# Optimization experiments

Measured on AMD Instinct MI355X. Metric: run time of the kernel, lower is better.

Reference implementation:

```python
import jax, jax.numpy as jnp
import numpy as np

H, K, V, F = 8, 64, 192, 192  # heads, key_size, value_size, num_position_features


def central_mask_features(distances, feature_size, seq_length):
    # distances: [L] float; returns [L, feature_size]
    pow_rate = np.exp(np.log(seq_length + 1) / feature_size).astype('float32')
    center_widths = jnp.power(pow_rate, jnp.arange(1, feature_size + 1, dtype=jnp.float32)) - 1.0
    return (center_widths[None, :] > jnp.abs(distances)[:, None]).astype(jnp.float32)


def positional_features(distances, feature_size, seq_length, symmetric=False):
    num_components = 1 if symmetric else 2
    emb = central_mask_features(distances, feature_size // num_components, seq_length)
    if not symmetric:
        emb = jnp.concatenate([emb, jnp.sign(distances)[:, None] * emb], axis=-1)
    return emb  # [L, feature_size]


def relative_shift(x):
    # x: [B, H, T1, T2] with T2 = 2*T1 - 1 -> [B, H, T1, T1]
    b, h, t1, t2 = x.shape
    x = jnp.pad(x, ((0, 0), (0, 0), (0, 0), (1, 0)))  # [B,H,T1,T2+1]
    x = x.reshape(b, h, t2 + 1, t1)[:, :, 1:, :]      # drop first row
    x = x.reshape(b, h, t1, t2)
    return x[..., : (t2 + 1) // 2]


def setup_inputs() -> dict:
    key = jax.random.key(0)
    ks = jax.random.split(key, 9)
    B, T, C = 2, 1536, 1536
    s = 1.0 / np.sqrt(C).astype('float32')
    return {
        'inputs': jax.random.normal(ks[0], (B, T, C), jnp.float32),
        'Wq': jax.random.normal(ks[1], (C, H * K), jnp.float32) * s,
        'Wk': jax.random.normal(ks[2], (C, H * K), jnp.float32) * s,
        'Wv': jax.random.normal(ks[3], (C, H * V), jnp.float32) * s,
        'Wrk': jax.random.normal(ks[4], (F, H * K), jnp.float32) * (1.0 / np.sqrt(F).astype('float32')),
        'We': jax.random.normal(ks[5], (H * V, H * V), jnp.float32) * (1.0 / np.sqrt(H * V).astype('float32')),
        'be': jnp.zeros((H * V,), jnp.float32),
        'r_w_bias': jax.random.normal(ks[6], (1, H, 1, K), jnp.float32) * 0.1,
        'r_r_bias': jax.random.normal(ks[7], (1, H, 1, K), jnp.float32) * 0.1,
    }


def reference(inputs, Wq, Wk, Wv, Wrk, We, be, r_w_bias, r_r_bias):
    B, T, C = inputs.shape

    def heads(x, d):  # [B,T,H*d] -> [B,H,T,d]
        return x.reshape(B, T, H, d).transpose(0, 2, 1, 3)

    q = heads(inputs @ Wq, K) * (K ** -0.5)
    k = heads(inputs @ Wk, K)
    v = heads(inputs @ Wv, V)

    # content logits: (q + r_w_bias) k^T -> [B,H,T,T]
    content_logits = jnp.einsum('bhqk,bhmk->bhqm', q + r_w_bias, k)

    # relative position logits
    distances = jnp.arange(-T + 1, T, dtype=jnp.float32)  # [2T-1]
    pe = positional_features(distances, F, T, symmetric=False)  # [2T-1, F]
    r_k = (pe @ Wrk).reshape(2 * T - 1, H, K).transpose(1, 0, 2)  # [H, 2T-1, K]
    rel_logits = jnp.einsum('bhqk,hmk->bhqm', q + r_r_bias, r_k)  # [B,H,T,2T-1]
    rel_logits = relative_shift(rel_logits)  # [B,H,T,T]

    logits = content_logits + rel_logits
    attn = jax.nn.softmax(logits, axis=-1)
    out = jnp.einsum('bhqm,bhmv->bhqv', attn, v)  # [B,H,T,V]
    out = out.transpose(0, 2, 1, 3).reshape(B, T, H * V)
    return out @ We + be
```

## Files before the change

kernel.cpp:

```cpp
#include <hip/hip_runtime.h>
#include <math.h>

#define HB 8
#define KD 64
#define VD 192
#define BT 2
#define TT 1536
#define CC 1536
#define HK (HB*KD)
#define HV (HB*VD)
#define QKVP 2560
#define LOG2E 1.44269504088896340736f

typedef float f32x4 __attribute__((ext_vector_type(4)));
typedef __bf16 bf16x8 __attribute__((ext_vector_type(8)));

static __device__ __forceinline__ ushort f2bf(float f) {
  union { float f; uint u; } v; v.f = f;
  uint r = (v.u + 0x7FFFu + ((v.u >> 16) & 1u)) >> 16;
  return (ushort)r;
}
static __device__ __forceinline__ float bf2f(ushort u) {
  union { uint u; float f; } v; v.u = ((uint)u) << 16; return v.f;
}

static __device__ __forceinline__ f32x4 mfma_bf(bf16x8 a, bf16x8 b, f32x4 c) {
  return __builtin_amdgcn_mfma_f32_16x16x32_bf16(a, b, c, 0, 0, 0);
}

static __device__ __forceinline__ void gload_lds16(const ushort* g, ushort* l) {
  __builtin_amdgcn_global_load_lds(
      (const __attribute__((address_space(1))) unsigned int*)g,
      (__attribute__((address_space(3))) unsigned int*)l, 16, 0, 0);
}

__device__ __forceinline__ void storeC(float* p, float v) { *p = v; }
__device__ __forceinline__ void storeC(ushort* p, float v) { *p = f2bf(v); }

__global__ __launch_bounds__(256) void cast_bf16(
    const float* __restrict__ in, ushort* __restrict__ out, int n4)
{
  for (int i = blockIdx.x*blockDim.x + threadIdx.x; i < n4; i += gridDim.x*blockDim.x) {
    float4 v = ((const float4*)in)[i];
    ushort4 o; o.x = f2bf(v.x); o.y = f2bf(v.y); o.z = f2bf(v.z); o.w = f2bf(v.w);
    ((ushort4*)out)[i] = o;
  }
}

__global__ void tcast(const float* __restrict__ in, ushort* __restrict__ out, int R, int C, float scale)
{
  __shared__ float tile[32][33];
  const int bx = blockIdx.x * 32;
  const int by = blockIdx.y * 32;
  const int tx = threadIdx.x, ty = threadIdx.y;
  #pragma unroll
  for (int i = 0; i < 4; ++i)
    tile[ty + i*8][tx] = in[(size_t)(by + ty + i*8)*C + bx + tx];
  __syncthreads();
  #pragma unroll
  for (int i = 0; i < 4; ++i)
    out[(size_t)(bx + ty + i*8)*R + by + tx] = f2bf(tile[tx][ty + i*8] * scale);
}

__global__ void vtrans(const ushort* __restrict__ in, ushort* __restrict__ out)
{
  __shared__ ushort tile[32][33];
  const int bx = blockIdx.x * 32;
  const int by = blockIdx.y * 32;
  const int tx = threadIdx.x, ty = threadIdx.y;
  #pragma unroll
  for (int i = 0; i < 4; ++i)
    tile[ty + i*8][tx] = in[(size_t)(by + ty + i*8)*QKVP + 1024 + bx + tx];
  __syncthreads();
  #pragma unroll
  for (int i = 0; i < 4; ++i)
    out[(size_t)(bx + ty + i*8)*(BT*TT) + by + tx] = tile[tx][ty + i*8];
}

template<bool WITH_BIAS, typename OutT>
__global__ __launch_bounds__(256) void gemm_bf16(
    const ushort* __restrict__ A, const ushort* __restrict__ Bt,
    const float* __restrict__ bias, OutT* __restrict__ C,
    int M, int N, int Kd)
{
  __shared__ __align__(16) ushort As[128*64];
  __shared__ __align__(16) ushort Bs[128*64];
  const int t = threadIdx.x;
  const int w = t >> 6, lane = t & 63;
  const int lrow = lane & 15, lk8 = lane >> 4;
  const int row0 = blockIdx.y * 128, col0 = blockIdx.x * 128;
  const int wr = (w >> 1) * 64, wc = (w & 1) * 64;

  f32x4 acc[4][4];
  #pragma unroll
  for (int m = 0; m < 4; ++m)
    #pragma unroll
    for (int n = 0; n < 4; ++n) acc[m][n] = (f32x4){0.f,0.f,0.f,0.f};

  for (int k0 = 0; k0 < Kd; k0 += 64) {
    __syncthreads();
    #pragma unroll
    for (int j = 0; j < 4; ++j) {
      const int c = (w*4 + j)*64 + lane;
      const int r = c >> 3, cp = c & 7;
      const int sc = cp ^ (r & 7);
      gload_lds16(A  + (size_t)(row0 + r)*Kd + k0 + sc*8, As + c*8);
      gload_lds16(Bt + (size_t)(col0 + r)*Kd + k0 + sc*8, Bs + c*8);
    }
    __syncthreads();
    bf16x8 af[4][2], bfv[4][2];
    #pragma unroll
    for (int m = 0; m < 4; ++m) {
      const int r = wr + m*16 + lrow;
      #pragma unroll
      for (int kh = 0; kh < 2; ++kh) {
        const int k8 = lk8 + kh*4;
        af[m][kh] = *(const bf16x8*)&As[r*64 + ((k8 ^ (r & 7)) << 3)];
      }
    }
    #pragma unroll
    for (int n = 0; n < 4; ++n) {
      const int r = wc + n*16 + lrow;
      #pragma unroll
      for (int kh = 0; kh < 2; ++kh) {
        const int k8 = lk8 + kh*4;
        bfv[n][kh] = *(const bf16x8*)&Bs[r*64 + ((k8 ^ (r & 7)) << 3)];
      }
    }
    #pragma unroll
    for (int m = 0; m < 4; ++m)
      #pragma unroll
      for (int n = 0; n < 4; ++n) {
        acc[m][n] = mfma_bf(af[m][0], bfv[n][0], acc[m][n]);
        acc[m][n] = mfma_bf(af[m][1], bfv[n][1], acc[m][n]);
      }
  }
  #pragma unroll
  for (int m = 0; m < 4; ++m)
    #pragma unroll
    for (int n = 0; n < 4; ++n) {
      const int cg = col0 + wc + n*16 + lrow;
      const float bb = WITH_BIAS ? bias[cg] : 0.f;
      #pragma unroll
      for (int r = 0; r < 4; ++r) {
        const int rg = row0 + wr + m*16 + lk8*4 + r;
        storeC(&C[(size_t)rg*N + cg], acc[m][n][r] + bb);
      }
    }
}

__global__ __launch_bounds__(256) void wrk_suffix(
    const float* __restrict__ Wrk, float* __restrict__ S1, float* __restrict__ S2)
{
  const int c = blockIdx.x*blockDim.x + threadIdx.x;
  float a1 = 0.f, a2 = 0.f;
  S1[96*HK + c] = 0.f; S2[96*HK + c] = 0.f;
  for (int i = 95; i >= 0; --i) {
    a1 += Wrk[i*HK + c];
    a2 += Wrk[(96 + i)*HK + c];
    S1[i*HK + c] = a1; S2[i*HK + c] = a2;
  }
}

__global__ __launch_bounds__(256) void relk_fill(
    const float* __restrict__ S1, const float* __restrict__ S2,
    const float* __restrict__ rrb, ushort* __restrict__ rk, float* __restrict__ c2g)
{
  __shared__ float cw[96];
  __shared__ float red[512];
  __shared__ int i0s;
  const int t = threadIdx.x;
  const int m = blockIdx.x;
  if (t < 96) {
    double pr = exp(log((double)(TT + 1)) / 96.0);
    float prf = (float)pr;
    cw[t] = (float)pow((double)prf, (double)(t + 1)) - 1.0f;
  }
  __syncthreads();
  const int d = m - (TT - 1);
  const float ad = fabsf((float)d);
  if (t == 0) {
    int i0 = 96;
    for (int i = 0; i < 96; ++i) if (cw[i] > ad) { i0 = i; break; }
    i0s = i0;
  }
  __syncthreads();
  const float sg = (d > 0) ? 1.f : (d < 0 ? -1.f : 0.f);
  const int i0 = i0s;
  for (int c = t; c < HK; c += 256) {
    const float val = S1[i0*HK + c] + sg * S2[i0*HK + c];
    const ushort vb = f2bf(val);
    rk[(size_t)m * HK + c] = vb;
    red[c] = bf2f(vb) * rrb[c];
  }
  __syncthreads();
  if (t < 8) {
    float s = 0.f;
    #pragma unroll 16
    for (int i = 0; i < 64; ++i) s += red[t*64 + i];
    c2g[(size_t)t*(2*TT - 1) + m] = s * LOG2E;
  }
}

__global__ __launch_bounds__(256) void c1_kernel(
    const ushort* __restrict__ qkv, const float* __restrict__ rwb, float* __restrict__ c1g)
{
  const int idx = blockIdx.x*256 + threadIdx.x;
  const int h = idx & 7, row = idx >> 3;
  const ushort* kr = &qkv[(size_t)row*QKVP + 512 + h*KD];
  float s = 0.f;
  #pragma unroll 16
  for (int c = 0; c < 64; ++c) s += bf2f(kr[c]) * rwb[h*KD + c];
  c1g[h*(BT*TT) + row] = s * LOG2E;
}

__global__ __launch_bounds__(256, 2) void attn_mfma(
    const ushort* __restrict__ qkv, const ushort* __restrict__ vTg,
    const ushort* __restrict__ rk,
    const float* __restrict__ c1g, const float* __restrict__ c2g,
    ushort* __restrict__ aout)
{
  __shared__ __align__(16) ushort ktL[64*64];
  __shared__ __align__(16) ushort rkbL[96*64];
  __shared__ __align__(16) ushort vTl[192*64];
  __shared__ __align__(16) ushort Pl[32][72];
  __shared__ __align__(16) float S1[32][68];
  __shared__ __align__(16) float S2[32][98];
  __shared__ float corrl[32], linv[32];

  const int t = threadIdx.x;
  const int wv = t >> 6, lane = t & 63;
  const int lrow = lane & 15, lk8 = lane >> 4;
  const int bid = blockIdx.x;
  const int qt = bid % (TT/32);
  const int h  = (bid / (TT/32)) % HB;
  const int b  = bid / ((TT/32) * HB);
  const int q0 = qt * 32;

  bf16x8 af00, af01, af10, af11;
  {
    const ushort* qbase = &qkv[((size_t)(b*TT) + q0 + lrow)*QKVP + h*KD];
    af00 = *(const bf16x8*)&qbase[lk8*8];
    af01 = *(const bf16x8*)&qbase[32 + lk8*8];
    af10 = *(const bf16x8*)&qbase[16*QKVP + lk8*8];
    af11 = *(const bf16x8*)&qbase[16*QKVP + 32 + lk8*8];
  }

  if (t < 32) ((uint*)rkbL)[95*32 + t] = 0;

  const ushort* ksrc[2]; ushort* kdst[2];
  #pragma unroll
  for (int W = 0; W < 2; ++W) {
    const int c = W*256 + t;
    const int r = c >> 3, cp = c & 7;
    ksrc[W] = qkv + (size_t)(b*TT + r)*QKVP + 512 + h*KD + (cp ^ (r & 7))*8;
    kdst[W] = ktL + c*8;
  }
  const ushort* rsrc[3]; ushort* rdst[3];
  #pragma unroll
  for (int W = 0; W < 3; ++W) {
    const int c = W*256 + t;
    const int r = c >> 3, cp = c & 7;
    rsrc[W] = rk + (size_t)(1504 - q0 + r)*HK + h*KD + (cp ^ (r & 7))*8;
    rdst[W] = rkbL + c*8;
  }
  const bool rval = t < 248;
  const ushort* vsrc[6]; ushort* vdst[6];
  #pragma unroll
  for (int W = 0; W < 6; ++W) {
    const int c = W*256 + t;
    const int vd = c >> 3, cpk = c & 7;
    vsrc[W] = vTg + (size_t)(h*VD + vd)*(BT*TT) + b*TT + (cpk ^ (vd & 7))*8;
    vdst[W] = vTl + c*8;
  }

  int jk_[2], rt1_[2], j2_[3], rt2_[3];
  #pragma unroll
  for (int s = 0; s < 2; ++s) {
    const int idx = wv*2 + s;
    rt1_[s] = idx >> 2; jk_[s] = (idx & 3)*16 + lrow;
  }
  #pragma unroll
  for (int s = 0; s < 3; ++s) {
    const int idx = wv*3 + s;
    rt2_[s] = (idx >= 6) ? 1 : 0; j2_[s] = (idx - 6*rt2_[s])*16 + lrow;
  }

  f32x4 acc[2][3];
  #pragma unroll
  for (int i = 0; i < 2; ++i)
    #pragma unroll
    for (int j = 0; j < 3; ++j) acc[i][j] = (f32x4){0.f, 0.f, 0.f, 0.f};
  float m_i = -1e30f, l_i = 0.f;
  const int r_s = t >> 3;
  const int vsl = t & 7;

  float c1p[2], c2p[3];
  {
    const int mb0 = -q0 + 1504;
    #pragma unroll
    for (int s = 0; s < 2; ++s) c1p[s] = c1g[h*(BT*TT) + b*TT + jk_[s]];
    #pragma unroll
    for (int s = 0; s < 3; ++s) {
      const float v = c2g[(size_t)h*(2*TT - 1) + mb0 + (j2_[s] < 95 ? j2_[s] : 94)];
      c2p[s] = (j2_[s] < 95) ? v : 0.f;
    }
  }
  #pragma unroll
  for (int W = 0; W < 2; ++W) { gload_lds16(ksrc[W], kdst[W]); ksrc[W] += 64*QKVP; }
  gload_lds16(rsrc[0], rdst[0]);           rsrc[0] += 64*HK;
  gload_lds16(rsrc[1], rdst[1]);           rsrc[1] += 64*HK;
  if (rval) gload_lds16(rsrc[2], rdst[2]);
  rsrc[2] += 64*HK;
  #pragma unroll
  for (int W = 0; W < 6; ++W) { gload_lds16(vsrc[W], vdst[W]); vsrc[W] += 64; }

  for (int it = 0; it < 24; ++it) {
    asm volatile("s_waitcnt vmcnt(6)" ::: "memory");
    __builtin_amdgcn_s_barrier();
    #pragma unroll
    for (int s = 0; s < 2; ++s) {
      const int rt = rt1_[s], jk = jk_[s];
      const bf16x8 a0 = rt ? af10 : af00;
      const bf16x8 a1 = rt ? af11 : af01;
      bf16x8 b0 = *(const bf16x8*)&ktL[jk*64 + ((lk8 ^ (jk & 7)) << 3)];
      bf16x8 b1 = *(const bf16x8*)&ktL[jk*64 + (((lk8 + 4) ^ (jk & 7)) << 3)];
      f32x4 c0 = (f32x4){0.f, 0.f, 0.f, 0.f};
      c0 = mfma_bf(a0, b0, c0);
      c0 = mfma_bf(a1, b1, c0);
      #pragma unroll
      for (int r = 0; r < 4; ++r) S1[rt*16 + lk8*4 + r][jk] = c0[r] + c1p[s];
    }
    #pragma unroll
    for (int s = 0; s < 3; ++s) {
      const int rt = rt2_[s], j2 = j2_[s];
      const bf16x8 a0 = rt ? af10 : af00;
      const bf16x8 a1 = rt ? af11 : af01;
      bf16x8 b0 = *(const bf16x8*)&rkbL[j2*64 + ((lk8 ^ (j2 & 7)) << 3)];
      bf16x8 b1 = *(const bf16x8*)&rkbL[j2*64 + (((lk8 + 4) ^ (j2 & 7)) << 3)];
      f32x4 c0 = (f32x4){0.f, 0.f, 0.f, 0.f};
      c0 = mfma_bf(a0, b0, c0);
      c0 = mfma_bf(a1, b1, c0);
      #pragma unroll
      for (int r = 0; r < 4; ++r) S2[rt*16 + lk8*4 + r][j2] = c0[r] + c2p[s];
    }
    asm volatile("s_waitcnt lgkmcnt(0)" ::: "memory");
    __builtin_amdgcn_s_barrier();

    if (it < 23) {
      #pragma unroll
      for (int W = 0; W < 2; ++W) { gload_lds16(ksrc[W], kdst[W]); ksrc[W] += 64*QKVP; }
      gload_lds16(rsrc[0], rdst[0]);           rsrc[0] += 64*HK;
      gload_lds16(rsrc[1], rdst[1]);           rsrc[1] += 64*HK;
      if (rval) gload_lds16(rsrc[2], rdst[2]);
      rsrc[2] += 64*HK;
      const int kt0n = (it + 1) << 6;
      const int mbn = kt0n - q0 + 1504;
      #pragma unroll
      for (int s = 0; s < 2; ++s) c1p[s] = c1g[h*(BT*TT) + b*TT + kt0n + jk_[s]];
      #pragma unroll
      for (int s = 0; s < 3; ++s) {
        const float v = c2g[(size_t)h*(2*TT - 1) + mbn + (j2_[s] < 95 ? j2_[s] : 94)];
        c2p[s] = (j2_[s] < 95) ? v : 0.f;
      }
    }
    {
      float sv[8];
      #pragma unroll
      for (int i = 0; i < 8; ++i) {
        const int j = vsl*8 + i;
        sv[i] = S1[r_s][j] + S2[r_s][j - r_s + 31];
      }
      float lmax = sv[0];
      #pragma unroll
      for (int i = 1; i < 8; ++i) lmax = fmaxf(lmax, sv[i]);
      #pragma unroll
      for (int s = 1; s < 8; s <<= 1) lmax = fmaxf(lmax, __shfl_xor(lmax, s, 64));
      const bool defer = (lmax <= m_i + 8.0f);
      const float m_new = defer ? m_i : fmaxf(m_i, lmax);
      const float corr  = defer ? 1.0f : exp2f(m_i - m_new);
      float p[8];
      float lsum = 0.f;
      #pragma unroll
      for (int i = 0; i < 8; ++i) { p[i] = exp2f(sv[i] - m_new); lsum += p[i]; }
      uint4 pw;
      pw.x = (uint)f2bf(p[0]) | ((uint)f2bf(p[1]) << 16);
      pw.y = (uint)f2bf(p[2]) | ((uint)f2bf(p[3]) << 16);
      pw.z = (uint)f2bf(p[4]) | ((uint)f2bf(p[5]) << 16);
      pw.w = (uint)f2bf(p[6]) | ((uint)f2bf(p[7]) << 16);
      *(uint4*)&Pl[r_s][vsl*8] = pw;
      #pragma unroll
      for (int s = 1; s < 8; s <<= 1) lsum += __shfl_xor(lsum, s, 64);
      l_i = l_i * corr + lsum;
      m_i = m_new;
      if (vsl == 0) corrl[r_s] = corr;
    }
    if (it < 23) { asm volatile("s_waitcnt vmcnt(10)" ::: "memory"); }
    else         { asm volatile("s_waitcnt vmcnt(0)"  ::: "memory"); }
    asm volatile("s_waitcnt lgkmcnt(0)" ::: "memory");
    __builtin_amdgcn_s_barrier();

    {
      bf16x8 pa[2][2], bv[3][2];
      #pragma unroll
      for (int rt = 0; rt < 2; ++rt) {
        pa[rt][0] = *(const bf16x8*)&Pl[rt*16 + lrow][lk8*8];
        pa[rt][1] = *(const bf16x8*)&Pl[rt*16 + lrow][32 + lk8*8];
      }
      #pragma unroll
      for (int cc = 0; cc < 3; ++cc) {
        const int rv = (3*wv + cc)*16 + lrow;
        bv[cc][0] = *(const bf16x8*)&vTl[rv*64 + ((lk8 ^ (rv & 7)) << 3)];
        bv[cc][1] = *(const bf16x8*)&vTl[rv*64 + (((lk8 + 4) ^ (rv & 7)) << 3)];
      }
      float cr[2][4];
      #pragma unroll
      for (int rt = 0; rt < 2; ++rt)
        #pragma unroll
        for (int r = 0; r < 4; ++r) cr[rt][r] = corrl[rt*16 + lk8*4 + r];
      asm volatile("s_waitcnt lgkmcnt(0)" ::: "memory");
      __builtin_amdgcn_s_barrier();
      if (it < 23) {
        #pragma unroll
        for (int W = 0; W < 6; ++W) { gload_lds16(vsrc[W], vdst[W]); vsrc[W] += 64; }
      }
      bool need = false;
      #pragma unroll
      for (int rt = 0; rt < 2; ++rt)
        #pragma unroll
        for (int r = 0; r < 4; ++r) need |= (cr[rt][r] != 1.0f);
      if (__any(need ? 1 : 0)) {
        #pragma unroll
        for (int rt = 0; rt < 2; ++rt)
          #pragma unroll
          for (int cc = 0; cc < 3; ++cc)
            #pragma unroll
            for (int r = 0; r < 4; ++r) acc[rt][cc][r] *= cr[rt][r];
      }
      #pragma unroll
      for (int rt = 0; rt < 2; ++rt)
        #pragma unroll
        for (int cc = 0; cc < 3; ++cc) {
          acc[rt][cc] = mfma_bf(pa[rt][0], bv[cc][0], acc[rt][cc]);
          acc[rt][cc] = mfma_bf(pa[rt][1], bv[cc][1], acc[rt][cc]);
        }
    }
  }
  if (vsl == 0) linv[r_s] = 1.0f / l_i;
  __syncthreads();
  #pragma unroll
  for (int rt = 0; rt < 2; ++rt) {
    #pragma unroll
    for (int cc = 0; cc < 3; ++cc) {
      const int colg = (3*wv + cc)*16 + lrow;
      #pragma unroll
      for (int r = 0; r < 4; ++r) {
        const int rowg = rt*16 + lk8*4 + r;
        aout[((size_t)(b*TT) + q0 + rowg) * HV + h*VD + colg] = f2bf(acc[rt][cc][r] * linv[rowg]);
      }
    }
  }
}

extern "C" void kernel_launch(void* const* d_in, const int* in_sizes, int n_in,
                              void* d_out, int out_size, void* d_ws, size_t ws_size,
                              hipStream_t stream)
{
  const float* X   = (const float*)d_in[0];
  const float* Wq  = (const float*)d_in[1];
  const float* Wk  = (const float*)d_in[2];
  const float* Wv  = (const float*)d_in[3];
  const float* Wrk = (const float*)d_in[4];
  const float* We  = (const float*)d_in[5];
  const float* be  = (const float*)d_in[6];
  const float* rwb = (const float*)d_in[7];
  const float* rrb = (const float*)d_in[8];
  float* out = (float*)d_out;

  char* ws = (char*)d_ws;
  ushort* Xb    = (ushort*)ws;                       ws += (size_t)3072*1536*2;
  ushort* Wqkvt = (ushort*)ws;                       ws += (size_t)2560*1536*2;
  ushort* Wet   = (ushort*)ws;                       ws += (size_t)1536*1536*2;
  float*  S1b   = (float*)ws;                        ws += (size_t)97*512*4;
  float*  S2b   = (float*)ws;                        ws += (size_t)97*512*4;
  ushort* qkvb  = (ushort*)ws;                       ws += (size_t)3072*2560*2;
  ushort* vTgb  = (ushort*)ws;                       ws += (size_t)1536*3072*2;
  ushort* rkb   = (ushort*)ws;                       ws += (size_t)3071*512*2;
  float*  c1g   = (float*)ws;                        ws += (size_t)8*3072*4;
  float*  c2g   = (float*)ws;                        ws += (size_t)8*3071*4;
  ushort* ao    = (ushort*)ws;

  dim3 blk(256);
  cast_bf16<<<2048, blk, 0, stream>>>(X, Xb, (3072*1536)/4);
  tcast<<<dim3(512/32, 1536/32),  dim3(32,8), 0, stream>>>(Wq, Wqkvt,                      1536, 512,  0.125f*LOG2E);
  tcast<<<dim3(512/32, 1536/32),  dim3(32,8), 0, stream>>>(Wk, Wqkvt + (size_t)512*1536,   1536, 512,  1.0f);
  tcast<<<dim3(1536/32, 1536/32), dim3(32,8), 0, stream>>>(Wv, Wqkvt + (size_t)1024*1536,  1536, 1536, 1.0f);
  tcast<<<dim3(1536/32, 1536/32), dim3(32,8), 0, stream>>>(We, Wet, 1536, 1536, 1.0f);
  wrk_suffix<<<2, blk, 0, stream>>>(Wrk, S1b, S2b);
  relk_fill<<<dim3(2*TT - 1), blk, 0, stream>>>(S1b, S2b, rrb, rkb, c2g);
  gemm_bf16<false, ushort><<<dim3(20, 24), blk, 0, stream>>>(Xb, Wqkvt, nullptr, qkvb, 3072, QKVP, 1536);
  vtrans<<<dim3(1536/32, 3072/32), dim3(32,8), 0, stream>>>(qkvb, vTgb);
  c1_kernel<<<96, blk, 0, stream>>>(qkvb, rwb, c1g);
  attn_mfma<<<dim3(BT*HB*(TT/32)), blk, 0, stream>>>(qkvb, vTgb, rkb, c1g, c2g, ao);
  gemm_bf16<true, float><<<dim3(12, 24), blk, 0, stream>>>(ao, Wet, be, out, 3072, 1536, 1536);
}
```

Baseline: 217.9 us.

## Load attention MFMA operands directly from global memory instead of LDS staging

The attention kernel no longer stages K, relative-key and V tiles in shared memory through async global-to-LDS prefetch. MFMA B-operands are now read straight from global memory each iteration, and the LDS footprint shrinks to the score, probability and correction buffers. Launch bounds rise from 2 to 4 blocks per CU so more waves can hide latency. The cost is the loss of the software-pipelined prefetch, more redundant global/L2 traffic across waves, and fully exposed load latency within each iteration.

```diff
diff --git a/kernel.cpp b/kernel.cpp
--- a/kernel.cpp
+++ b/kernel.cpp
@@ -214,18 +214,15 @@
   c1g[h*(BT*TT) + row] = s * LOG2E;
 }
 
-__global__ __launch_bounds__(256, 2) void attn_mfma(
+__global__ __launch_bounds__(256, 4) void attn_mfma(
     const ushort* __restrict__ qkv, const ushort* __restrict__ vTg,
     const ushort* __restrict__ rk,
     const float* __restrict__ c1g, const float* __restrict__ c2g,
     ushort* __restrict__ aout)
 {
-  __shared__ __align__(16) ushort ktL[64*64];
-  __shared__ __align__(16) ushort rkbL[96*64];
-  __shared__ __align__(16) ushort vTl[192*64];
-  __shared__ __align__(16) ushort Pl[32][72];
   __shared__ __align__(16) float S1[32][68];
   __shared__ __align__(16) float S2[32][98];
+  __shared__ __align__(16) ushort Pl[32][72];
   __shared__ float corrl[32], linv[32];
 
   const int t = threadIdx.x;
@@ -246,34 +243,6 @@
     af11 = *(const bf16x8*)&qbase[16*QKVP + 32 + lk8*8];
   }
 
-  if (t < 32) ((uint*)rkbL)[95*32 + t] = 0;
-
-  const ushort* ksrc[2]; ushort* kdst[2];
-  #pragma unroll
-  for (int W = 0; W < 2; ++W) {
-    const int c = W*256 + t;
-    const int r = c >> 3, cp = c & 7;
-    ksrc[W] = qkv + (size_t)(b*TT + r)*QKVP + 512 + h*KD + (cp ^ (r & 7))*8;
-    kdst[W] = ktL + c*8;
-  }
-  const ushort* rsrc[3]; ushort* rdst[3];
-  #pragma unroll
-  for (int W = 0; W < 3; ++W) {
-    const int c = W*256 + t;
-    const int r = c >> 3, cp = c & 7;
-    rsrc[W] = rk + (size_t)(1504 - q0 + r)*HK + h*KD + (cp ^ (r & 7))*8;
-    rdst[W] = rkbL + c*8;
-  }
-  const bool rval = t < 248;
-  const ushort* vsrc[6]; ushort* vdst[6];
-  #pragma unroll
-  for (int W = 0; W < 6; ++W) {
-    const int c = W*256 + t;
-    const int vd = c >> 3, cpk = c & 7;
-    vsrc[W] = vTg + (size_t)(h*VD + vd)*(BT*TT) + b*TT + (cpk ^ (vd & 7))*8;
-    vdst[W] = vTl + c*8;
-  }
-
   int jk_[2], rt1_[2], j2_[3], rt2_[3];
   #pragma unroll
   for (int s = 0; s < 2; ++s) {
@@ -285,6 +254,10 @@
     const int idx = wv*3 + s;
     rt2_[s] = (idx >= 6) ? 1 : 0; j2_[s] = (idx - 6*rt2_[s])*16 + lrow;
   }
+
+  const ushort* kbase = qkv + (size_t)(b*TT)*QKVP + 512 + h*KD;
+  const ushort* rbase = rk + (size_t)(1504 - q0)*HK + h*KD;
+  const ushort* vbase = vTg + (size_t)(h*VD)*(BT*TT) + b*TT;
 
   f32x4 acc[2][3];
   #pragma unroll
@@ -295,36 +268,25 @@
   const int r_s = t >> 3;
   const int vsl = t & 7;
 
-  float c1p[2], c2p[3];
-  {
-    const int mb0 = -q0 + 1504;
-    #pragma unroll
-    for (int s = 0; s < 2; ++s) c1p[s] = c1g[h*(BT*TT) + b*TT + jk_[s]];
+  for (int it = 0; it < 24; ++it) {
+    const int kt0 = it << 6;
+    const int mb = kt0 - q0 + 1504;
+    float c1p[2], c2p[3];
+    #pragma unroll
+    for (int s = 0; s < 2; ++s) c1p[s] = c1g[h*(BT*TT) + b*TT + kt0 + jk_[s]];
     #pragma unroll
     for (int s = 0; s < 3; ++s) {
-      const float v = c2g[(size_t)h*(2*TT - 1) + mb0 + (j2_[s] < 95 ? j2_[s] : 94)];
+      const float v = c2g[(size_t)h*(2*TT - 1) + (kt0 - q0 + 1504) + (j2_[s] < 95 ? j2_[s] : 94)];
       c2p[s] = (j2_[s] < 95) ? v : 0.f;
     }
-  }
-  #pragma unroll
-  for (int W = 0; W < 2; ++W) { gload_lds16(ksrc[W], kdst[W]); ksrc[W] += 64*QKVP; }
-  gload_lds16(rsrc[0], rdst[0]);           rsrc[0] += 64*HK;
-  gload_lds16(rsrc[1], rdst[1]);           rsrc[1] += 64*HK;
-  if (rval) gload_lds16(rsrc[2], rdst[2]);
-  rsrc[2] += 64*HK;
-  #pragma unroll
-  for (int W = 0; W < 6; ++W) { gload_lds16(vsrc[W], vdst[W]); vsrc[W] += 64; }
-
-  for (int it = 0; it < 24; ++it) {
-    asm volatile("s_waitcnt vmcnt(6)" ::: "memory");
-    __builtin_amdgcn_s_barrier();
     #pragma unroll
     for (int s = 0; s < 2; ++s) {
       const int rt = rt1_[s], jk = jk_[s];
+      const ushort* kr = kbase + (size_t)(kt0 + jk)*QKVP;
+      bf16x8 b0 = *(const bf16x8*)&kr[lk8*8];
+      bf16x8 b1 = *(const bf16x8*)&kr[32 + lk8*8];
       const bf16x8 a0 = rt ? af10 : af00;
       const bf16x8 a1 = rt ? af11 : af01;
-      bf16x8 b0 = *(const bf16x8*)&ktL[jk*64 + ((lk8 ^ (jk & 7)) << 3)];
-      bf16x8 b1 = *(const bf16x8*)&ktL[jk*64 + (((lk8 + 4) ^ (jk & 7)) << 3)];
       f32x4 c0 = (f32x4){0.f, 0.f, 0.f, 0.f};
       c0 = mfma_bf(a0, b0, c0);
       c0 = mfma_bf(a1, b1, c0);
@@ -334,36 +296,19 @@
     #pragma unroll
     for (int s = 0; s < 3; ++s) {
       const int rt = rt2_[s], j2 = j2_[s];
+      const int grow = kt0 + (j2 < 95 ? j2 : 94);
+      const ushort* rr = rbase + (size_t)grow*HK;
+      bf16x8 b0 = *(const bf16x8*)&rr[lk8*8];
+      bf16x8 b1 = *(const bf16x8*)&rr[32 + lk8*8];
       const bf16x8 a0 = rt ? af10 : af00;
       const bf16x8 a1 = rt ? af11 : af01;
-      bf16x8 b0 = *(const bf16x8*)&rkbL[j2*64 + ((lk8 ^ (j2 & 7)) << 3)];
-      bf16x8 b1 = *(const bf16x8*)&rkbL[j2*64 + (((lk8 + 4) ^ (j2 & 7)) << 3)];
       f32x4 c0 = (f32x4){0.f, 0.f, 0.f, 0.f};
       c0 = mfma_bf(a0, b0, c0);
       c0 = mfma_bf(a1, b1, c0);
       #pragma unroll
       for (int r = 0; r < 4; ++r) S2[rt*16 + lk8*4 + r][j2] = c0[r] + c2p[s];
     }
-    asm volatile("s_waitcnt lgkmcnt(0)" ::: "memory");
-    __builtin_amdgcn_s_barrier();
-
-    if (it < 23) {
-      #pragma unroll
-      for (int W = 0; W < 2; ++W) { gload_lds16(ksrc[W], kdst[W]); ksrc[W] += 64*QKVP; }
-      gload_lds16(rsrc[0], rdst[0]);           rsrc[0] += 64*HK;
-      gload_lds16(rsrc[1], rdst[1]);           rsrc[1] += 64*HK;
-      if (rval) gload_lds16(rsrc[2], rdst[2]);
-      rsrc[2] += 64*HK;
-      const int kt0n = (it + 1) << 6;
-      const int mbn = kt0n - q0 + 1504;
-      #pragma unroll
-      for (int s = 0; s < 2; ++s) c1p[s] = c1g[h*(BT*TT) + b*TT + kt0n + jk_[s]];
-      #pragma unroll
-      for (int s = 0; s < 3; ++s) {
-        const float v = c2g[(size_t)h*(2*TT - 1) + mbn + (j2_[s] < 95 ? j2_[s] : 94)];
-        c2p[s] = (j2_[s] < 95) ? v : 0.f;
-      }
-    }
+    __syncthreads();
     {
       float sv[8];
       #pragma unroll
@@ -395,11 +340,7 @@
       m_i = m_new;
       if (vsl == 0) corrl[r_s] = corr;
     }
-    if (it < 23) { asm volatile("s_waitcnt vmcnt(10)" ::: "memory"); }
-    else         { asm volatile("s_waitcnt vmcnt(0)"  ::: "memory"); }
-    asm volatile("s_waitcnt lgkmcnt(0)" ::: "memory");
-    __builtin_amdgcn_s_barrier();
-
+    __syncthreads();
     {
       bf16x8 pa[2][2], bv[3][2];
       #pragma unroll
@@ -410,20 +351,15 @@
       #pragma unroll
       for (int cc = 0; cc < 3; ++cc) {
         const int rv = (3*wv + cc)*16 + lrow;
-        bv[cc][0] = *(const bf16x8*)&vTl[rv*64 + ((lk8 ^ (rv & 7)) << 3)];
-        bv[cc][1] = *(const bf16x8*)&vTl[rv*64 + (((lk8 + 4) ^ (rv & 7)) << 3)];
+        const ushort* vr = vbase + (size_t)rv*(BT*TT) + kt0;
+        bv[cc][0] = *(const bf16x8*)&vr[lk8*8];
+        bv[cc][1] = *(const bf16x8*)&vr[32 + lk8*8];
       }
       float cr[2][4];
       #pragma unroll
       for (int rt = 0; rt < 2; ++rt)
         #pragma unroll
         for (int r = 0; r < 4; ++r) cr[rt][r] = corrl[rt*16 + lk8*4 + r];
-      asm volatile("s_waitcnt lgkmcnt(0)" ::: "memory");
-      __builtin_amdgcn_s_barrier();
-      if (it < 23) {
-        #pragma unroll
-        for (int W = 0; W < 6; ++W) { gload_lds16(vsrc[W], vdst[W]); vsrc[W] += 64; }
-      }
       bool need = false;
       #pragma unroll
       for (int rt = 0; rt < 2; ++rt)
```

After: 283.5 us. +30.1%, slower.
